# Kernel optimization log

Measured on AMD Instinct MI355X. Metric: run time of the kernel, lower is better.

The kernel has to match this reference:

```python
import jax, jax.numpy as jnp
import numpy as np

N, D, C = 4096, 2048, 128
MARGIN = 0.3


def _choice(key, mask):
    # Uniform random choice among True entries of mask (Gumbel-max trick).
    g = jax.random.gumbel(key, mask.shape, jnp.float32)
    return jnp.argmax(jnp.where(mask, g, -jnp.inf))


def setup_inputs() -> dict:
    key = jax.random.key(0)
    k1, k2, k3, k4, k5 = jax.random.split(key, 5)
    return {
        "inputs": jax.random.normal(k1, (N, D), jnp.float32),
        "prediction": jax.random.normal(k2, (N, C), jnp.float32),
        "targets": jax.random.randint(k3, (N,), 0, C),
        "true_targets": jax.random.randint(k4, (N,), 0, C),
        "prob": jax.random.uniform(k5, (N,), jnp.float32),
        "threshold": jnp.float32(0.5),
    }


def _forward(inputs, prediction, prob, threshold, targets, true_targets):
    n = inputs.shape[0]
    # Pairwise Euclidean distances: ||xi||^2 + ||xj||^2 - 2 xi.xj  (clamped, sqrt)
    sq = jnp.sum(inputs * inputs, axis=1)
    dist = jnp.sqrt(jnp.clip(sq[:, None] + sq[None, :] - 2.0 * (inputs @ inputs.T), 1e-12, None))
    is_pos = targets[:, None] == targets[None, :]
    confident = prob >= threshold
    pred_cls = jnp.argmax(prediction, axis=1)

    # 12 closest negatives per row (rank 0 = hardest; ranks 1..11 cover the
    # original's fallback loop of at most 10 extra steps, j in 1..11).
    neg_dist = jnp.where(is_pos, jnp.inf, dist)
    _, neg_rank = jax.lax.top_k(-neg_dist, 12)  # [n, 12] indices

    row_keys = jax.random.split(jax.random.key(42), n)
    idx = jnp.arange(n)

    def per_row(i, rk):
        di = dist[i]
        pos_mask = is_pos[i]
        kp, kr = jax.random.split(rk)
        rp = _choice(kp, pos_mask & (idx != i))  # random positive != anchor
        hn = neg_rank[i, 0]                      # hardest negative
        ap0, an0 = di[rp], di[hn]
        p_pos = prob[rp] >= threshold
        p_neg = prob[hn] >= threshold
        is_FN = pred_cls[hn] == targets[i]

        # Case B (pos confident, neg unconfident, false-negative):
        # first confident negative among ranks 1..11, else rank 11.
        cand = neg_rank[i, 1:12]
        conf_c = prob[cand] >= threshold
        hn_new = cand[jnp.where(jnp.any(conf_c), jnp.argmax(conf_c), 10)]
        apB, anB = (ap0 + an0) * 0.5, di[hn_new]

        # Cases C / D-not-FN: resample positive, up to 6 draws total,
        # first draw that is confident and != anchor, else the last draw.
        draws = jax.vmap(lambda k: _choice(k, pos_mask))(jax.random.split(kr, 6))
        valid = (draws != i) & (prob[draws] >= threshold)
        rp_new = draws[jnp.where(jnp.any(valid), jnp.argmax(valid), 5)]
        apC, anC = di[rp_new], (ap0 + an0) * 0.5

        useB = p_pos & ~p_neg & is_FN
        useC = (~p_pos & p_neg) | (~p_pos & ~p_neg & ~is_FN)
        inverse = ~p_pos & ~p_neg & is_FN  # keep ap0/an0, flip hinge direction

        ap = jnp.where(useB, apB, jnp.where(useC, apC, ap0))
        an = jnp.where(useB, anB, jnp.where(useC, anC, an0))
        per_loss = jnp.where(inverse,
                             jnp.maximum(an - ap + MARGIN, 0.0),
                             jnp.maximum(ap - an + MARGIN, 0.0))
        return ap, an, per_loss

    aps, ans, losses = jax.vmap(per_row)(idx, row_keys)
    cnt = jnp.sum(confident)
    loss_sum = jnp.sum(jnp.where(confident, losses, 0.0))
    loss = jnp.where(cnt > 0, loss_sum / jnp.maximum(cnt, 1).astype(loss_sum.dtype),
                     jnp.zeros((), loss_sum.dtype))
    correct = jnp.sum(confident & (ans >= aps))
    return loss, correct, cnt


def reference(inputs, prediction, targets, true_targets, prob, threshold):
    return _forward(inputs, prediction, prob, threshold, targets, true_targets)
```

## Files before the change

kernel.cpp:

```cpp
#include <hip/hip_runtime.h>
#include <hip/hip_bf16.h>
#include <cstdint>
#include <cmath>

#define NROWS 4096
#define DIM   2048
#define CNUM  128
#define MARGIN_F 0.3f
#define TOPK 12
#define MAXM 256
#define GBK 32
#define CAP 160

#define BM 64
#define BN 64
#define BK 16
#define SLICES 8
#define COLS_PER_SLICE (NROWS / SLICES)

typedef _Float16 f16x8 __attribute__((ext_vector_type(8)));
typedef float    f32x4 __attribute__((ext_vector_type(4)));

#define GLD_LDS16(g, l)                                                        \
    __builtin_amdgcn_global_load_lds(                                          \
        (const __attribute__((address_space(1))) uint32_t*)(g),                \
        (__attribute__((address_space(3))) uint32_t*)(l), 16, 0, 0)

__device__ __forceinline__ uint32_t rnd_u32(uint32_t row, uint32_t k) {
    uint64_t x = ((uint64_t)row << 32) ^ (0x9E3779B97F4A7C15ULL * (uint64_t)(k + 1u));
    x ^= x >> 33; x *= 0xff51afd7ed558ccdULL;
    x ^= x >> 33; x *= 0xc4ceb9fe1a85ec53ULL;
    x ^= x >> 33;
    return (uint32_t)x;
}

__global__ void rowsq_kernel(const float* __restrict__ X, float* __restrict__ sq) {
    int wave = (blockIdx.x * blockDim.x + threadIdx.x) >> 6;
    int lane = threadIdx.x & 63;
    if (wave >= NROWS) return;
    const float4* xp = (const float4*)(X + (size_t)wave * DIM);
    float s = 0.f;
    for (int k = lane; k < DIM / 4; k += 64) {
        float4 v = xp[k];
        s += v.x * v.x + v.y * v.y + v.z * v.z + v.w * v.w;
    }
    for (int off = 32; off; off >>= 1) s += __shfl_xor(s, off, 64);
    if (lane == 0) sq[wave] = s;
}

__global__ void prep_kernel(const float* __restrict__ X, _Float16* __restrict__ Xh,
                            float* __restrict__ sq) {
    __shared__ float ws[4];
    int row = blockIdx.x, tid = threadIdx.x;
    int wave = tid >> 6, lane = tid & 63;
    const float4* xp = (const float4*)(X + (size_t)row * DIM);
    float4 a = xp[tid * 2], b = xp[tid * 2 + 1];
    float s = a.x * a.x + a.y * a.y + a.z * a.z + a.w * a.w
            + b.x * b.x + b.y * b.y + b.z * b.z + b.w * b.w;
    _Float16 h[8] = { (_Float16)a.x, (_Float16)a.y, (_Float16)a.z, (_Float16)a.w,
                      (_Float16)b.x, (_Float16)b.y, (_Float16)b.z, (_Float16)b.w };
    ((uint4*)(Xh + (size_t)row * DIM))[tid] = *(uint4*)h;
    for (int off = 32; off; off >>= 1) s += __shfl_xor(s, off, 64);
    if (lane == 0) ws[wave] = s;
    __syncthreads();
    if (tid == 0) sq[row] = ws[0] + ws[1] + ws[2] + ws[3];
}

__global__ void predcls_kernel(const float* __restrict__ P, int* __restrict__ cls) {
    int row = (blockIdx.x * blockDim.x + threadIdx.x) >> 6;
    int lane = threadIdx.x & 63;
    if (row >= NROWS) return;
    const float* p = P + (size_t)row * CNUM;
    float v0 = p[lane]; int i0 = lane;
    float v1 = p[lane + 64];
    if (v1 > v0) { v0 = v1; i0 = lane + 64; }
    for (int off = 1; off < 64; off <<= 1) {
        float ov = __shfl_xor(v0, off, 64);
        int   oi = __shfl_xor(i0, off, 64);
        if (ov > v0 || (ov == v0 && oi < i0)) { v0 = ov; i0 = oi; }
    }
    if (lane == 0) cls[row] = i0;
}

__global__ void classlist_kernel(const int* __restrict__ tgt,
                                 int* __restrict__ cnt, int* __restrict__ members) {
    int c = (blockIdx.x * blockDim.x + threadIdx.x) >> 6;
    int lane = threadIdx.x & 63;
    if (c >= CNUM) return;
    int k = 0;
    for (int base = 0; base < NROWS; base += 64) {
        int i = base + lane;
        bool m = (tgt[i] == c);
        unsigned long long mask = __ballot(m);
        if (m) {
            int pos = k + __popcll(mask & ((1ull << lane) - 1ull));
            if (pos < MAXM) members[c * MAXM + pos] = i;
        }
        k += __popcll(mask);
    }
    if (lane == 0) cnt[c] = (k < MAXM) ? k : MAXM;
}

__launch_bounds__(256, 4)
__global__ void mfma_dist_kernel(const _Float16* __restrict__ Xh,
                                 const float* __restrict__ sq, const int* __restrict__ tgt,
                                 float* __restrict__ dist) {
    __shared__ _Float16 Ah[2][128 * GBK];
    __shared__ _Float16 Bh[2][128 * GBK];
    __shared__ float    trb[4][16 * 17];
    __shared__ float    sqA[128], sqB[128];
    __shared__ int      tgA[128], tgB[128];

    int b = blockIdx.x;
    int br = 0, S = 0;
    while (b >= S + (32 - br)) { S += 32 - br; br++; }
    int bc = br + (b - S);

    int r0 = br * 128, c0 = bc * 128;
    int tid = threadIdx.x;
    int wave = tid >> 6, lane = tid & 63;
    int wr = wave >> 1, wc = wave & 1;

    if (tid < 128) { sqA[tid] = sq[r0 + tid]; tgA[tid] = tgt[r0 + tid]; }
    else { int t = tid - 128; sqB[t] = sq[c0 + t]; tgB[t] = tgt[c0 + t]; }

    f32x4 acc[4][4];
#pragma unroll
    for (int i = 0; i < 4; i++)
#pragma unroll
        for (int j = 0; j < 4; j++) acc[i][j] = (f32x4)0.f;

    const _Float16* gA[2]; const _Float16* gB[2];
    int ldsOff[2];
#pragma unroll
    for (int q = 0; q < 2; q++) {
        int rl = wave * 32 + q * 16 + (lane >> 2);
        int slot = lane & 3;
        int c = (slot - ((rl >> 1) & 3)) & 3;
        gA[q] = Xh + (size_t)(r0 + rl) * DIM + c * 8;
        gB[q] = Xh + (size_t)(c0 + rl) * DIM + c * 8;
        ldsOff[q] = (wave * 32 + q * 16) * GBK;
    }

    auto stage = [&](int buf, int kOff) {
#pragma unroll
        for (int q = 0; q < 2; q++) {
            GLD_LDS16(gA[q] + kOff, &Ah[buf][ldsOff[q]]);
            GLD_LDS16(gB[q] + kOff, &Bh[buf][ldsOff[q]]);
        }
    };

    stage(0, 0);
    int fr = lane & 15, fq = lane >> 4;

    for (int it = 0; it < DIM / GBK; it++) {
        int cur = it & 1;
        __syncthreads();
        if (it + 1 < DIM / GBK) stage(cur ^ 1, (it + 1) * GBK);
        f16x8 af[4], bf[4];
#pragma unroll
        for (int i = 0; i < 4; i++) {
            int row = wr * 64 + i * 16 + fr;
            int slot = (fq + ((row >> 1) & 3)) & 3;
            af[i] = *(const f16x8*)&Ah[cur][row * GBK + slot * 8];
        }
#pragma unroll
        for (int j = 0; j < 4; j++) {
            int col = wc * 64 + j * 16 + fr;
            int slot = (fq + ((col >> 1) & 3)) & 3;
            bf[j] = *(const f16x8*)&Bh[cur][col * GBK + slot * 8];
        }
#pragma unroll
        for (int i = 0; i < 4; i++)
#pragma unroll
            for (int j = 0; j < 4; j++)
                acc[i][j] = __builtin_amdgcn_mfma_f32_16x16x32_f16(af[i], bf[j], acc[i][j], 0, 0, 0);
    }

    float* tb = trb[wave];
#pragma unroll
    for (int i = 0; i < 4; i++) {
#pragma unroll
        for (int j = 0; j < 4; j++) {
            int lcol = wc * 64 + j * 16 + fr;
            float d[4];
#pragma unroll
            for (int r = 0; r < 4; r++) {
                int lrow = wr * 64 + i * 16 + fq * 4 + r;
                float v = sqA[lrow] + sqB[lcol] - 2.f * acc[i][j][r];
                if (tgA[lrow] == tgB[lcol]) v = INFINITY;
                d[r] = v;
                __builtin_nontemporal_store(v, &dist[(size_t)(r0 + lrow) * NROWS + (c0 + lcol)]);
            }
            if (br != bc) {
#pragma unroll
                for (int r = 0; r < 4; r++) tb[fr * 17 + fq * 4 + r] = d[r];
#pragma unroll
                for (int r = 0; r < 4; r++) {
                    float v = tb[(fq * 4 + r) * 17 + fr];
                    int grow = c0 + wc * 64 + j * 16 + fq * 4 + r;
                    int gcol = r0 + wr * 64 + i * 16 + fr;
                    __builtin_nontemporal_store(v, &dist[(size_t)grow * NROWS + gcol]);
                }
            }
        }
    }
}

__launch_bounds__(256)
__global__ void topk_kernel(const float* __restrict__ dist,
                            float* __restrict__ top_v, int* __restrict__ top_i) {
    __shared__ float cbv[4][CAP];
    __shared__ int   cbi[4][CAP];
    int wave = threadIdx.x >> 6, lane = threadIdx.x & 63;
    int row = blockIdx.x * 4 + wave;
    const f32x4* d = (const f32x4*)(dist + (size_t)row * NROWS);

    f32x4 v[16];
#pragma unroll
    for (int t = 0; t < 16; t++) v[t] = __builtin_nontemporal_load(&d[t * 64 + lane]);

    float lmin = INFINITY, lmax = -INFINITY, lsum = 0.f;
    int lcnt = 0;
#pragma unroll
    for (int t = 0; t < 16; t++) {
#pragma unroll
        for (int c = 0; c < 4; c++) {
            float x = v[t][c];
            bool fin = x < INFINITY;
            lmin = fminf(lmin, x);
            lmax = fmaxf(lmax, fin ? x : -INFINITY);
            lsum += fin ? x : 0.f;
            lcnt += fin ? 1 : 0;
        }
    }
    for (int off = 32; off; off >>= 1) {
        lmin = fminf(lmin, __shfl_xor(lmin, off, 64));
        lmax = fmaxf(lmax, __shfl_xor(lmax, off, 64));
        lsum += __shfl_xor(lsum, off, 64);
        lcnt += __shfl_xor(lcnt, off, 64);
    }
    float mu = lsum / (float)(lcnt > 0 ? lcnt : 1);

    float lo = lmin, hi = lmax + 1.0f;
    float tau = lmin + 0.3f * (mu - lmin);
    if (!(tau > lo && tau < hi)) tau = 0.5f * (lo + hi);
    for (int it = 0; it < 32; it++) {
        int lc = 0;
#pragma unroll
        for (int t = 0; t < 16; t++) {
            lc += (v[t][0] < tau) + (v[t][1] < tau) + (v[t][2] < tau) + (v[t][3] < tau);
        }
        for (int off = 32; off; off >>= 1) lc += __shfl_xor(lc, off, 64);
        if (lc >= TOPK && lc <= CAP) break;
        if (lc < TOPK) lo = tau; else hi = tau;
        tau = 0.5f * (lo + hi);
    }

    int cnt = 0;
#pragma unroll
    for (int t = 0; t < 16; t++) {
#pragma unroll
        for (int c = 0; c < 4; c++) {
            float x = v[t][c];
            bool p = x < tau;
            unsigned long long mk = __ballot(p);
            if (p) {
                int pos = cnt + __popcll(mk & ((1ull << lane) - 1ull));
                if (pos < CAP) {
                    cbv[wave][pos] = x;
                    cbi[wave][pos] = (t * 64 + lane) * 4 + c;
                }
            }
            cnt += __popcll(mk);
        }
    }
    if (cnt > CAP) cnt = CAP;

    float mv[3]; int mi[3];
#pragma unroll
    for (int r = 0; r < 3; r++) {
        int p = r * 64 + lane;
        bool ok = p < cnt;
        mv[r] = ok ? cbv[wave][p] : INFINITY;
        mi[r] = ok ? cbi[wave][p] : 0x7FFFFFFF;
    }

    for (int t = 0; t < TOPK; t++) {
        float bv = mv[0]; int bi = mi[0];
        if (mv[1] < bv || (mv[1] == bv && mi[1] < bi)) { bv = mv[1]; bi = mi[1]; }
        if (mv[2] < bv || (mv[2] == bv && mi[2] < bi)) { bv = mv[2]; bi = mi[2]; }
        for (int off = 32; off; off >>= 1) {
            float ov = __shfl_xor(bv, off, 64);
            int   oi = __shfl_xor(bi, off, 64);
            if (ov < bv || (ov == bv && oi < bi)) { bv = ov; bi = oi; }
        }
        if (lane == 0) {
            top_v[(size_t)row * TOPK + t] = bv;
            int si = (bi >= 0 && bi < NROWS) ? bi : 0;
            top_i[(size_t)row * TOPK + t] = si;
        }
#pragma unroll
        for (int r = 0; r < 3; r++)
            if (mi[r] == bi) { mv[r] = INFINITY; mi[r] = 0x7FFFFFFF; }
    }
}

__launch_bounds__(256)
__global__ void dist_topk_kernel(const float* __restrict__ X, const float* __restrict__ sq,
                                 const int* __restrict__ tgt,
                                 float* __restrict__ part_v, int* __restrict__ part_i) {
    __shared__ float As[BK][BM];
    __shared__ float Bs[BK][BN];
    __shared__ float Cs[BM][BN + 1];
    __shared__ float sqA[BM], sqB[BN];
    __shared__ int   tgA[BM], tgB[BN];

    int rowBase = blockIdx.x * BM;
    int slice = blockIdx.y;
    int tid = threadIdx.x;
    int tx = tid & 15, ty = tid >> 4;

    if (tid < BM) { sqA[tid] = sq[rowBase + tid]; tgA[tid] = tgt[rowBase + tid]; }

    float lv[TOPK]; int li[TOPK];
#pragma unroll
    for (int k = 0; k < TOPK; k++) { lv[k] = INFINITY; li[k] = -1; }

    for (int jt = 0; jt < COLS_PER_SLICE / BN; jt++) {
        int colBase = slice * COLS_PER_SLICE + jt * BN;
        __syncthreads();
        if (tid < BN) { sqB[tid] = sq[colBase + tid]; tgB[tid] = tgt[colBase + tid]; }

        float acc[4][4] = {};
        for (int kb = 0; kb < DIM; kb += BK) {
            int r  = tid >> 2;
            int kk = (tid & 3) * 4;
            float4 va = *(const float4*)(X + (size_t)(rowBase + r) * DIM + kb + kk);
            As[kk + 0][r] = va.x; As[kk + 1][r] = va.y; As[kk + 2][r] = va.z; As[kk + 3][r] = va.w;
            float4 vb = *(const float4*)(X + (size_t)(colBase + r) * DIM + kb + kk);
            Bs[kk + 0][r] = vb.x; Bs[kk + 1][r] = vb.y; Bs[kk + 2][r] = vb.z; Bs[kk + 3][r] = vb.w;
            __syncthreads();
#pragma unroll
            for (int k = 0; k < BK; k++) {
                float a[4], b2[4];
                *(float4*)a = *(const float4*)&As[k][ty * 4];
                *(float4*)b2 = *(const float4*)&Bs[k][tx * 4];
#pragma unroll
                for (int i2 = 0; i2 < 4; i2++)
#pragma unroll
                    for (int j2 = 0; j2 < 4; j2++)
                        acc[i2][j2] += a[i2] * b2[j2];
            }
            __syncthreads();
        }
#pragma unroll
        for (int i2 = 0; i2 < 4; i2++) {
            int r = ty * 4 + i2;
#pragma unroll
            for (int j2 = 0; j2 < 4; j2++) {
                int c = tx * 4 + j2;
                float d2 = sqA[r] + sqB[c] - 2.f * acc[i2][j2];
                if (tgA[r] == tgB[c]) d2 = INFINITY;
                Cs[r][c] = d2;
            }
        }
        __syncthreads();
        if (tid < BM) {
            int r = tid;
            for (int c = 0; c < BN; c++) {
                float v = Cs[r][c];
                if (v < lv[TOPK - 1]) {
                    float nv = v; int ni = colBase + c;
#pragma unroll
                    for (int p = 0; p < TOPK; p++) {
                        if (nv < lv[p]) {
                            float tv = lv[p]; int ti = li[p];
                            lv[p] = nv; li[p] = ni;
                            nv = tv; ni = ti;
                        }
                    }
                }
            }
        }
    }
    if (tid < BM) {
        int r = tid;
#pragma unroll
        for (int k = 0; k < TOPK; k++) {
            size_t o = ((size_t)(rowBase + r) * SLICES + slice) * TOPK + k;
            part_v[o] = lv[k];
            part_i[o] = li[k];
        }
    }
}

__global__ void topk_merge_kernel(const float* __restrict__ part_v, const int* __restrict__ part_i,
                                  float* __restrict__ top_v, int* __restrict__ top_i) {
    int row = blockIdx.x * blockDim.x + threadIdx.x;
    if (row >= NROWS) return;
    float lv[TOPK]; int li[TOPK];
#pragma unroll
    for (int k = 0; k < TOPK; k++) { lv[k] = INFINITY; li[k] = -1; }
    for (int s = 0; s < SLICES; s++) {
        for (int k = 0; k < TOPK; k++) {
            size_t o = ((size_t)row * SLICES + s) * TOPK + k;
            float v = part_v[o];
            if (!(v < lv[TOPK - 1])) break;
            int idx = part_i[o];
            float nv = v; int ni = idx;
#pragma unroll
            for (int p = 0; p < TOPK; p++) {
                if (nv < lv[p]) {
                    float tv = lv[p]; int ti = li[p];
                    lv[p] = nv; li[p] = ni;
                    nv = tv; ni = ti;
                }
            }
        }
    }
#pragma unroll
    for (int k = 0; k < TOPK; k++) {
        top_v[(size_t)row * TOPK + k] = lv[k];
        top_i[(size_t)row * TOPK + k] = li[k];
    }
}

__global__ void rowlogic_kernel(const float* __restrict__ X, const float* __restrict__ sq,
                                const float* __restrict__ prob, const float* __restrict__ thr_p,
                                const int* __restrict__ tgt, const int* __restrict__ pred_cls,
                                const int* __restrict__ class_cnt, const int* __restrict__ class_mem,
                                const float* __restrict__ top_v, const int* __restrict__ top_i,
                                float* __restrict__ row_loss, int* __restrict__ row_corr) {
    int i = (blockIdx.x * blockDim.x + threadIdx.x) >> 6;
    int lane = threadIdx.x & 63;
    if (i >= NROWS) return;
    float thr = *thr_p;

    int c = tgt[i];
    int cc = class_cnt[c];
    const int* mem = class_mem + c * MAXM;

    int pos_i = 0;
    for (int k = 0; k < cc; k++) { if (mem[k] == i) { pos_i = k; break; } }

    int rp = 0;
    if (cc > 1) {
        uint32_t r = rnd_u32((uint32_t)i, 0x9111u) % (uint32_t)(cc - 1);
        if ((int)r >= pos_i) r++;
        rp = mem[r];
    }

    int hn = top_i[(size_t)i * TOPK + 0];
    float an0 = sqrtf(fmaxf(top_v[(size_t)i * TOPK + 0], 1e-12f));
    bool p_neg = prob[hn] >= thr;
    bool is_FN = (pred_cls[hn] == c);

    int sel = 11;
    for (int k = 1; k <= 11; k++) {
        int cd = top_i[(size_t)i * TOPK + k];
        if (prob[cd] >= thr) { sel = k; break; }
    }
    float anB = sqrtf(fmaxf(top_v[(size_t)i * TOPK + sel], 1e-12f));

    int first_valid = -1, last_draw = 0;
    for (int k = 0; k < 6; k++) {
        uint32_t r = rnd_u32((uint32_t)i, 0xD000u + (uint32_t)k) % (uint32_t)(cc > 0 ? cc : 1);
        int dk = mem[r];
        last_draw = dk;
        if (first_valid < 0 && dk != i && prob[dk] >= thr) first_valid = dk;
    }
    int rp_new = (first_valid >= 0) ? first_valid : last_draw;
    bool p_pos = prob[rp] >= thr;

    const float4* xi = (const float4*)(X + (size_t)i * DIM);
    const float4* xr = (const float4*)(X + (size_t)rp * DIM);
    const float4* xn = (const float4*)(X + (size_t)rp_new * DIM);
    float s1 = 0.f, s2 = 0.f;
    for (int k = lane; k < DIM / 4; k += 64) {
        float4 a = xi[k], b = xr[k], d = xn[k];
        s1 += a.x * b.x + a.y * b.y + a.z * b.z + a.w * b.w;
        s2 += a.x * d.x + a.y * d.y + a.z * d.z + a.w * d.w;
    }
    for (int off = 32; off; off >>= 1) {
        s1 += __shfl_xor(s1, off, 64);
        s2 += __shfl_xor(s2, off, 64);
    }
    if (lane == 0) {
        float ap0 = sqrtf(fmaxf(sq[i] + sq[rp]     - 2.f * s1, 1e-12f));
        float apC = sqrtf(fmaxf(sq[i] + sq[rp_new] - 2.f * s2, 1e-12f));
        float apB = (ap0 + an0) * 0.5f;
        float anC = (ap0 + an0) * 0.5f;
        bool useB = p_pos && !p_neg && is_FN;
        bool useC = (!p_pos && p_neg) || (!p_pos && !p_neg && !is_FN);
        bool inverse = !p_pos && !p_neg && is_FN;
        float ap = useB ? apB : (useC ? apC : ap0);
        float an = useB ? anB : (useC ? anC : an0);
        float pl = inverse ? fmaxf(an - ap + MARGIN_F, 0.f)
                           : fmaxf(ap - an + MARGIN_F, 0.f);
        bool conf = prob[i] >= thr;
        row_loss[i] = conf ? pl : 0.f;
        row_corr[i] = (conf && (an >= ap)) ? 1 : 0;
    }
}

__global__ void reduce_kernel(const float* __restrict__ row_loss, const int* __restrict__ row_corr,
                              const float* __restrict__ prob, const float* __restrict__ thr_p,
                              float* __restrict__ out) {
    __shared__ float sl[256];
    __shared__ int   sc[256];
    __shared__ int   sn[256];
    float thr = *thr_p;
    int tid = threadIdx.x;
    float l = 0.f; int corr = 0, cnt = 0;
    for (int i = tid; i < NROWS; i += 256) {
        l += row_loss[i];
        corr += row_corr[i];
        cnt += (prob[i] >= thr) ? 1 : 0;
    }
    sl[tid] = l; sc[tid] = corr; sn[tid] = cnt;
    __syncthreads();
    for (int off = 128; off; off >>= 1) {
        if (tid < off) {
            sl[tid] += sl[tid + off];
            sc[tid] += sc[tid + off];
            sn[tid] += sn[tid + off];
        }
        __syncthreads();
    }
    if (tid == 0) {
        int cn = sn[0];
        float loss = (cn > 0) ? (sl[0] / (float)(cn > 1 ? cn : 1)) : 0.f;
        out[0] = loss;
        out[1] = (float)sc[0];
        out[2] = (float)cn;
    }
}

extern "C" void kernel_launch(void* const* d_in, const int* in_sizes, int n_in,
                              void* d_out, int out_size, void* d_ws, size_t ws_size,
                              hipStream_t stream) {
    const float* X    = (const float*)d_in[0];
    const float* P    = (const float*)d_in[1];
    const int*   tgt  = (const int*)d_in[2];
    const float* prob = (const float*)d_in[4];
    const float* thr  = (const float*)d_in[5];
    float* out = (float*)d_out;

    char* w = (char*)d_ws;
    auto alloc = [&](size_t bytes) {
        char* p = w;
        w += (bytes + 255) & ~(size_t)255;
        return p;
    };
    float* sq        = (float*)alloc(NROWS * sizeof(float));
    int*   pred_cls  = (int*)  alloc(NROWS * sizeof(int));
    int*   class_cnt = (int*)  alloc(CNUM * sizeof(int));
    int*   class_mem = (int*)  alloc((size_t)CNUM * MAXM * sizeof(int));
    float* top_v     = (float*)alloc((size_t)NROWS * TOPK * sizeof(float));
    int*   top_i     = (int*)  alloc((size_t)NROWS * TOPK * sizeof(int));
    float* row_loss  = (float*)alloc(NROWS * sizeof(float));
    int*   row_corr  = (int*)  alloc(NROWS * sizeof(int));
    char*  var_base  = w;

    size_t fast_need = (size_t)NROWS * DIM * 2 + (size_t)NROWS * NROWS * 4 + (1 << 20);
    bool fast = ((size_t)(var_base - (char*)d_ws) + fast_need) <= ws_size;

    predcls_kernel<<<NROWS / 4, 256, 0, stream>>>(P, pred_cls);
    classlist_kernel<<<CNUM / 4, 256, 0, stream>>>(tgt, class_cnt, class_mem);

    if (fast) {
        _Float16* Xh   = (_Float16*)alloc((size_t)NROWS * DIM * 2);
        float*    dist = (float*)alloc((size_t)NROWS * NROWS * 4);
        prep_kernel<<<NROWS, 256, 0, stream>>>(X, Xh, sq);
        mfma_dist_kernel<<<528, 256, 0, stream>>>(Xh, sq, tgt, dist);
        topk_kernel<<<NROWS / 4, 256, 0, stream>>>(dist, top_v, top_i);
    } else {
        rowsq_kernel<<<NROWS / 4, 256, 0, stream>>>(X, sq);
        float* part_v = (float*)alloc((size_t)NROWS * SLICES * TOPK * sizeof(float));
        int*   part_i = (int*)  alloc((size_t)NROWS * SLICES * TOPK * sizeof(int));
        dist_topk_kernel<<<dim3(NROWS / BM, SLICES), 256, 0, stream>>>(X, sq, tgt, part_v, part_i);
        topk_merge_kernel<<<NROWS / 256, 256, 0, stream>>>(part_v, part_i, top_v, top_i);
    }

    rowlogic_kernel<<<NROWS / 4, 256, 0, stream>>>(X, sq, prob, thr, tgt, pred_cls,
                                                   class_cnt, class_mem, top_v, top_i,
                                                   row_loss, row_corr);
    reduce_kernel<<<1, 256, 0, stream>>>(row_loss, row_corr, prob, thr, out);
}
```

Measured before the change: 230.8 us.

## Fuse per-tile top-k selection into MFMA distance kernel, drop full distance matrix

The MFMA distance kernel no longer writes the full 4096x4096 distance matrix. Each 128x128 tile is staged through shared memory, which aliases the GEMM operand buffers, and a per-thread insertion sort produces partial top-12 lists for both the tile rows and the mirrored rows. A new merge kernel combines the 64 partial lists per row. This removes the 64MB write and re-read of the distance matrix. The cost is serial insertion-sort work inside the GEMM kernel, with only half the threads active in diagonal tiles.

New measurement: 370.1 us. +60.3%, slower.

```diff
diff --git a/kernel.cpp b/kernel.cpp
--- a/kernel.cpp
+++ b/kernel.cpp
@@ -10,7 +10,6 @@
 #define TOPK 12
 #define MAXM 256
 #define GBK 32
-#define CAP 160
 
 #define BM 64
 #define BN 64
@@ -104,12 +103,10 @@
 __launch_bounds__(256, 4)
 __global__ void mfma_dist_kernel(const _Float16* __restrict__ Xh,
                                  const float* __restrict__ sq, const int* __restrict__ tgt,
-                                 float* __restrict__ dist) {
-    __shared__ _Float16 Ah[2][128 * GBK];
-    __shared__ _Float16 Bh[2][128 * GBK];
-    __shared__ float    trb[4][16 * 17];
-    __shared__ float    sqA[128], sqB[128];
-    __shared__ int      tgA[128], tgB[128];
+                                 float* __restrict__ part_v, int* __restrict__ part_i) {
+    __shared__ float Tls[64 * 129];
+    __shared__ float sqA[128], sqB[128];
+    __shared__ int   tgA[128], tgB[128];
 
     int b = blockIdx.x;
     int br = 0, S = 0;
@@ -129,6 +126,8 @@
     for (int i = 0; i < 4; i++)
 #pragma unroll
         for (int j = 0; j < 4; j++) acc[i][j] = (f32x4)0.f;
+
+    _Float16* AB = (_Float16*)Tls;
 
     const _Float16* gA[2]; const _Float16* gB[2];
     int ldsOff[2];
@@ -145,8 +144,8 @@
     auto stage = [&](int buf, int kOff) {
 #pragma unroll
         for (int q = 0; q < 2; q++) {
-            GLD_LDS16(gA[q] + kOff, &Ah[buf][ldsOff[q]]);
-            GLD_LDS16(gB[q] + kOff, &Bh[buf][ldsOff[q]]);
+            GLD_LDS16(gA[q] + kOff, AB + buf * 8192 + ldsOff[q]);
+            GLD_LDS16(gB[q] + kOff, AB + buf * 8192 + 4096 + ldsOff[q]);
         }
     };
 
@@ -157,18 +156,20 @@
         int cur = it & 1;
         __syncthreads();
         if (it + 1 < DIM / GBK) stage(cur ^ 1, (it + 1) * GBK);
+        const _Float16* Acur = AB + cur * 8192;
+        const _Float16* Bcur = Acur + 4096;
         f16x8 af[4], bf[4];
 #pragma unroll
         for (int i = 0; i < 4; i++) {
             int row = wr * 64 + i * 16 + fr;
             int slot = (fq + ((row >> 1) & 3)) & 3;
-            af[i] = *(const f16x8*)&Ah[cur][row * GBK + slot * 8];
+            af[i] = *(const f16x8*)&Acur[row * GBK + slot * 8];
         }
 #pragma unroll
         for (int j = 0; j < 4; j++) {
             int col = wc * 64 + j * 16 + fr;
             int slot = (fq + ((col >> 1) & 3)) & 3;
-            bf[j] = *(const f16x8*)&Bh[cur][col * GBK + slot * 8];
+            bf[j] = *(const f16x8*)&Bcur[col * GBK + slot * 8];
         }
 #pragma unroll
         for (int i = 0; i < 4; i++)
@@ -177,132 +178,96 @@
                 acc[i][j] = __builtin_amdgcn_mfma_f32_16x16x32_f16(af[i], bf[j], acc[i][j], 0, 0, 0);
     }
 
-    float* tb = trb[wave];
-#pragma unroll
-    for (int i = 0; i < 4; i++) {
-#pragma unroll
-        for (int j = 0; j < 4; j++) {
-            int lcol = wc * 64 + j * 16 + fr;
-            float d[4];
-#pragma unroll
-            for (int r = 0; r < 4; r++) {
-                int lrow = wr * 64 + i * 16 + fq * 4 + r;
-                float v = sqA[lrow] + sqB[lcol] - 2.f * acc[i][j][r];
-                if (tgA[lrow] == tgB[lcol]) v = INFINITY;
-                d[r] = v;
-                __builtin_nontemporal_store(v, &dist[(size_t)(r0 + lrow) * NROWS + (c0 + lcol)]);
-            }
-            if (br != bc) {
-#pragma unroll
-                for (int r = 0; r < 4; r++) tb[fr * 17 + fq * 4 + r] = d[r];
-#pragma unroll
-                for (int r = 0; r < 4; r++) {
-                    float v = tb[(fq * 4 + r) * 17 + fr];
-                    int grow = c0 + wc * 64 + j * 16 + fq * 4 + r;
-                    int gcol = r0 + wr * 64 + i * 16 + fr;
-                    __builtin_nontemporal_store(v, &dist[(size_t)grow * NROWS + gcol]);
+    for (int ph = 0; ph < 2; ph++) {
+        __syncthreads();
+        if (wr == ph) {
+#pragma unroll
+            for (int i = 0; i < 4; i++)
+#pragma unroll
+                for (int j = 0; j < 4; j++) {
+                    int lcol = wc * 64 + j * 16 + fr;
+#pragma unroll
+                    for (int r = 0; r < 4; r++) {
+                        int lrow = i * 16 + fq * 4 + r;
+                        float v = sqA[ph * 64 + lrow] + sqB[lcol] - 2.f * acc[i][j][r];
+                        if (tgA[ph * 64 + lrow] == tgB[lcol]) v = INFINITY;
+                        Tls[lrow * 129 + lcol] = v;
+                    }
+                }
+        }
+        __syncthreads();
+
+        float lv[TOPK]; int li[TOPK];
+#pragma unroll
+        for (int k = 0; k < TOPK; k++) { lv[k] = INFINITY; li[k] = 0x7FFFFFFF; }
+        int grow = 0, slot = 0, gcb = 0, start = 0, stride = 0;
+        bool active = false;
+        if (tid < 128) {
+            int lr = tid >> 1, h = tid & 1;
+            grow = r0 + ph * 64 + lr;
+            gcb  = c0 + h * 64;
+            slot = 2 * bc + h;
+            start = lr * 129 + h * 64; stride = 1;
+            active = true;
+        } else if (br != bc) {
+            int mr = tid - 128;
+            grow = c0 + mr;
+            gcb  = r0 + ph * 64;
+            slot = 2 * br + ph;
+            start = mr; stride = 129;
+            active = true;
+        }
+        if (active) {
+            for (int c = 0; c < 64; c++) {
+                float x = Tls[start + c * stride];
+                if (x < lv[TOPK - 1]) {
+                    float nv = x; int ni = gcb + c;
+#pragma unroll
+                    for (int p = 0; p < TOPK; p++) {
+                        if (nv < lv[p] || (nv == lv[p] && ni < li[p])) {
+                            float tv = lv[p]; int ti = li[p];
+                            lv[p] = nv; li[p] = ni; nv = tv; ni = ti;
+                        }
+                    }
                 }
             }
+            size_t o = ((size_t)grow * 64 + slot) * TOPK;
+#pragma unroll
+            for (int k = 0; k < TOPK; k++) { part_v[o + k] = lv[k]; part_i[o + k] = li[k]; }
         }
     }
 }
 
 __launch_bounds__(256)
-__global__ void topk_kernel(const float* __restrict__ dist,
-                            float* __restrict__ top_v, int* __restrict__ top_i) {
-    __shared__ float cbv[4][CAP];
-    __shared__ int   cbi[4][CAP];
+__global__ void topk_merge64_kernel(const float* __restrict__ part_v, const int* __restrict__ part_i,
+                                    float* __restrict__ top_v, int* __restrict__ top_i) {
+    __shared__ float sv[4][64 * TOPK];
+    __shared__ int   si[4][64 * TOPK];
     int wave = threadIdx.x >> 6, lane = threadIdx.x & 63;
     int row = blockIdx.x * 4 + wave;
-    const f32x4* d = (const f32x4*)(dist + (size_t)row * NROWS);
-
-    f32x4 v[16];
-#pragma unroll
-    for (int t = 0; t < 16; t++) v[t] = __builtin_nontemporal_load(&d[t * 64 + lane]);
-
-    float lmin = INFINITY, lmax = -INFINITY, lsum = 0.f;
-    int lcnt = 0;
-#pragma unroll
-    for (int t = 0; t < 16; t++) {
-#pragma unroll
-        for (int c = 0; c < 4; c++) {
-            float x = v[t][c];
-            bool fin = x < INFINITY;
-            lmin = fminf(lmin, x);
-            lmax = fmaxf(lmax, fin ? x : -INFINITY);
-            lsum += fin ? x : 0.f;
-            lcnt += fin ? 1 : 0;
-        }
-    }
-    for (int off = 32; off; off >>= 1) {
-        lmin = fminf(lmin, __shfl_xor(lmin, off, 64));
-        lmax = fmaxf(lmax, __shfl_xor(lmax, off, 64));
-        lsum += __shfl_xor(lsum, off, 64);
-        lcnt += __shfl_xor(lcnt, off, 64);
-    }
-    float mu = lsum / (float)(lcnt > 0 ? lcnt : 1);
-
-    float lo = lmin, hi = lmax + 1.0f;
-    float tau = lmin + 0.3f * (mu - lmin);
-    if (!(tau > lo && tau < hi)) tau = 0.5f * (lo + hi);
-    for (int it = 0; it < 32; it++) {
-        int lc = 0;
-#pragma unroll
-        for (int t = 0; t < 16; t++) {
-            lc += (v[t][0] < tau) + (v[t][1] < tau) + (v[t][2] < tau) + (v[t][3] < tau);
-        }
-        for (int off = 32; off; off >>= 1) lc += __shfl_xor(lc, off, 64);
-        if (lc >= TOPK && lc <= CAP) break;
-        if (lc < TOPK) lo = tau; else hi = tau;
-        tau = 0.5f * (lo + hi);
-    }
-
-    int cnt = 0;
-#pragma unroll
-    for (int t = 0; t < 16; t++) {
-#pragma unroll
-        for (int c = 0; c < 4; c++) {
-            float x = v[t][c];
-            bool p = x < tau;
-            unsigned long long mk = __ballot(p);
-            if (p) {
-                int pos = cnt + __popcll(mk & ((1ull << lane) - 1ull));
-                if (pos < CAP) {
-                    cbv[wave][pos] = x;
-                    cbi[wave][pos] = (t * 64 + lane) * 4 + c;
-                }
+    size_t base = (size_t)row * 64 * TOPK;
+    for (int k = lane; k < 64 * TOPK; k += 64) {
+        sv[wave][k] = part_v[base + k];
+        si[wave][k] = part_i[base + k];
+    }
+    int head = 0;
+    for (int t = 0; t < TOPK; t++) {
+        float hv = (head < TOPK) ? sv[wave][lane * TOPK + head] : INFINITY;
+        int   hi = (head < TOPK) ? si[wave][lane * TOPK + head] : 0x7FFFFFFF;
+        int   hl = lane;
+        for (int off = 32; off; off >>= 1) {
+            float ov = __shfl_xor(hv, off, 64);
+            int   oi = __shfl_xor(hi, off, 64);
+            int   ol = __shfl_xor(hl, off, 64);
+            if (ov < hv || (ov == hv && (oi < hi || (oi == hi && ol < hl)))) {
+                hv = ov; hi = oi; hl = ol;
             }
-            cnt += __popcll(mk);
-        }
-    }
-    if (cnt > CAP) cnt = CAP;
-
-    float mv[3]; int mi[3];
-#pragma unroll
-    for (int r = 0; r < 3; r++) {
-        int p = r * 64 + lane;
-        bool ok = p < cnt;
-        mv[r] = ok ? cbv[wave][p] : INFINITY;
-        mi[r] = ok ? cbi[wave][p] : 0x7FFFFFFF;
-    }
-
-    for (int t = 0; t < TOPK; t++) {
-        float bv = mv[0]; int bi = mi[0];
-        if (mv[1] < bv || (mv[1] == bv && mi[1] < bi)) { bv = mv[1]; bi = mi[1]; }
-        if (mv[2] < bv || (mv[2] == bv && mi[2] < bi)) { bv = mv[2]; bi = mi[2]; }
-        for (int off = 32; off; off >>= 1) {
-            float ov = __shfl_xor(bv, off, 64);
-            int   oi = __shfl_xor(bi, off, 64);
-            if (ov < bv || (ov == bv && oi < bi)) { bv = ov; bi = oi; }
         }
         if (lane == 0) {
-            top_v[(size_t)row * TOPK + t] = bv;
-            int si = (bi >= 0 && bi < NROWS) ? bi : 0;
-            top_i[(size_t)row * TOPK + t] = si;
-        }
-#pragma unroll
-        for (int r = 0; r < 3; r++)
-            if (mi[r] == bi) { mv[r] = INFINITY; mi[r] = 0x7FFFFFFF; }
+            top_v[(size_t)row * TOPK + t] = hv;
+            top_i[(size_t)row * TOPK + t] = (hi >= 0 && hi < NROWS) ? hi : 0;
+        }
+        if (lane == hl) head++;
     }
 }
 
@@ -563,7 +528,8 @@
     int*   row_corr  = (int*)  alloc(NROWS * sizeof(int));
     char*  var_base  = w;
 
-    size_t fast_need = (size_t)NROWS * DIM * 2 + (size_t)NROWS * NROWS * 4 + (1 << 20);
+    size_t fast_need = (size_t)NROWS * DIM * 2
+                     + 2 * ((size_t)NROWS * 64 * TOPK * 4) + (1 << 20);
     bool fast = ((size_t)(var_base - (char*)d_ws) + fast_need) <= ws_size;
 
     predcls_kernel<<<NROWS / 4, 256, 0, stream>>>(P, pred_cls);
@@ -571,10 +537,11 @@
 
     if (fast) {
         _Float16* Xh   = (_Float16*)alloc((size_t)NROWS * DIM * 2);
-        float*    dist = (float*)alloc((size_t)NROWS * NROWS * 4);
+        float* part_v  = (float*)alloc((size_t)NROWS * 64 * TOPK * sizeof(float));
+        int*   part_i  = (int*)  alloc((size_t)NROWS * 64 * TOPK * sizeof(int));
         prep_kernel<<<NROWS, 256, 0, stream>>>(X, Xh, sq);
-        mfma_dist_kernel<<<528, 256, 0, stream>>>(Xh, sq, tgt, dist);
-        topk_kernel<<<NROWS / 4, 256, 0, stream>>>(dist, top_v, top_i);
+        mfma_dist_kernel<<<528, 256, 0, stream>>>(Xh, sq, tgt, part_v, part_i);
+        topk_merge64_kernel<<<NROWS / 4, 256, 0, stream>>>(part_v, part_i, top_v, top_i);
     } else {
         rowsq_kernel<<<NROWS / 4, 256, 0, stream>>>(X, sq);
         float* part_v = (float*)alloc((size_t)NROWS * SLICES * TOPK * sizeof(float));
```
